# Performance work log

Measured on AMD Instinct MI355X. Metric: run time of the kernel, lower is better.

The kernel has to match this reference:

```python
import jax, jax.numpy as jnp
import numpy as np

B, S, V = 2, 336, 8      # batch, seq_len, n_vars
D, H, P = 256, 8, 96     # d_model, num_heads, pred_len
DK = D // H
OUT_CHN = 8
EPS = 1e-5


def _layernorm(x, g, b):
    mu = jnp.mean(x, axis=-1, keepdims=True)
    var = jnp.var(x, axis=-1, keepdims=True)
    return (x - mu) * jax.lax.rsqrt(var + EPS) * g + b


def _attn_ff(src, Wq, bq, Wk, bk, Wv, bv, Wo, bo, ln1_g, ln1_b):
    # src: [N, L, D]; manual MHA + residual + layernorm (dropout=0)
    N, L, _ = src.shape
    q = (src @ Wq + bq).reshape(N, L, H, DK).transpose(0, 2, 1, 3)
    k = (src @ Wk + bk).reshape(N, L, H, DK).transpose(0, 2, 1, 3)
    v = (src @ Wv + bv).reshape(N, L, H, DK).transpose(0, 2, 1, 3)
    scores = jnp.einsum('nhqd,nhkd->nhqk', q, k) / np.sqrt(DK).astype(np.float32)
    attn = jax.nn.softmax(scores, axis=-1)
    o = jnp.einsum('nhqk,nhkd->nhqd', attn, v)
    o = o.transpose(0, 2, 1, 3).reshape(N, L, D) @ Wo + bo
    return _layernorm(src + o, ln1_g, ln1_b)


def setup_inputs() -> dict:
    key = jax.random.key(0)
    ks = jax.random.split(key, 8)
    s = 1.0 / np.sqrt(D)
    return {
        'x': jax.random.normal(ks[0], (B, S, V), dtype=jnp.float32),
        'emb_w': jax.random.normal(ks[1], (1, D), dtype=jnp.float32),
        'emb_b': jnp.zeros((D,), jnp.float32),
        'Wq': jax.random.normal(ks[2], (D, D), dtype=jnp.float32) * s,
        'bq': jnp.zeros((D,), jnp.float32),
        'Wk': jax.random.normal(ks[3], (D, D), dtype=jnp.float32) * s,
        'bk': jnp.zeros((D,), jnp.float32),
        'Wv': jax.random.normal(ks[4], (D, D), dtype=jnp.float32) * s,
        'bv': jnp.zeros((D,), jnp.float32),
        'Wo': jax.random.normal(ks[5], (D, D), dtype=jnp.float32) * s,
        'bo': jnp.zeros((D,), jnp.float32),
        'ln1_g': jnp.ones((D,), jnp.float32),
        'ln1_b': jnp.zeros((D,), jnp.float32),
        'norm_g': jnp.ones((D,), jnp.float32),
        'norm_b': jnp.zeros((D,), jnp.float32),
        'proj_w': jax.random.normal(ks[6], (S * D, P), dtype=jnp.float32) / np.sqrt(S * D).astype(np.float32),
        'proj_b': jnp.zeros((P,), jnp.float32),
    }


def reference(x, emb_w, emb_b, Wq, bq, Wk, bk, Wv, bv, Wo, bo,
              ln1_g, ln1_b, norm_g, norm_b, proj_w, proj_b):
    attn_p = (Wq, bq, Wk, bk, Wv, bv, Wo, bo, ln1_g, ln1_b)
    # x: [B,S,V] -> [B,V,S] -> embed each scalar to D
    e = x.transpose(0, 2, 1)[..., None] @ emb_w + emb_b  # [B,V,S,D]
    for _ in range(10):
        # attention over time axis (shared weights)
        e = _attn_ff(e.reshape(B * V, S, D), *attn_p).reshape(B, V, S, D)
        e = _layernorm(e.transpose(0, 2, 1, 3), norm_g, norm_b)  # [B,S,V,D]
        # attention over variable axis (same weights)
        e = _attn_ff(e.reshape(B * S, V, D), *attn_p).reshape(B, S, V, D)
        e = e.transpose(0, 2, 1, 3)  # [B,V,S,D]
    out = e.reshape(B, V, S * D) @ proj_w + proj_b  # [B,V,P]
    return out.transpose(0, 2, 1)[:, :, :OUT_CHN]  # [B,P,out_chn]
```

## Files before the change

kernel.cpp:

```cpp
#include <hip/hip_runtime.h>

#define SS 336
#define VV 8
#define DD 256
#define DKK 32
#define NTOK 5376
#define NTD (NTOK * DD)
#define ATT_SCALE 0.17677669529663687f
#define LN_EPS 1e-5f

typedef _Float16 f16x8 __attribute__((ext_vector_type(8)));
typedef _Float16 f16x4v __attribute__((ext_vector_type(4)));
typedef __attribute__((ext_vector_type(4))) float f32x4;

__device__ inline _Float16 f2h(float f) { return (_Float16)f; }

__global__ __launch_bounds__(256) void k_init(
    const float* __restrict__ Wq, const float* __restrict__ Wk,
    const float* __restrict__ Wv, const float* __restrict__ Wo,
    const float* __restrict__ x, const float* __restrict__ ew,
    const float* __restrict__ eb, const float* __restrict__ PB,
    _Float16* __restrict__ WT2, float* __restrict__ E,
    _Float16* __restrict__ E16, float* __restrict__ out) {
  int bid = blockIdx.x;
  int tid = threadIdx.x;
  if (bid < 1024) {
    int z = bid >> 8;
    const float* W = (z == 0) ? Wq : (z == 1) ? Wk : (z == 2) ? Wv : Wo;
    int o = (bid & 255) * 256 + tid;
    int blk = o >> 9;
    int idx = o & 511;
    int lane = idx >> 3, j = idx & 7;
    int nt = blk >> 3, kb = blk & 7;
    int lcol = lane & 15, quad = lane >> 4;
    int n = nt * 16 + lcol;
    int k = kb * 32 + quad * 8 + j;
    WT2[(size_t)z * 65536 + o] = f2h(W[k * 256 + n]);
    if (bid == 0) {
      for (int i = tid; i < 1536; i += 256) {
        int row = i / 96, p = i - row * 96;
        out[(row >> 3) * 768 + p * 8 + (row & 7)] = PB[p];
      }
    }
  } else {
    int token = bid - 1024;
    int n = token / SS, s = token - n * SS;
    int b = n >> 3, v = n & 7;
    float xv = x[(b * SS + s) * VV + v];
    int d = tid;
    float val = fmaf(xv, ew[d], eb[d]);
    E[token * DD + d] = val;
    E16[token * DD + d] = f2h(val);
  }
}

#define KSTR 36
#define VTSTR 344
#define PSTR 72
#define QSTR 40
__global__ __launch_bounds__(512) void k_attn_time(
    const _Float16* __restrict__ Et16, const _Float16* __restrict__ Q16,
    const _Float16* __restrict__ K16, const _Float16* __restrict__ V16,
    const _Float16* __restrict__ WT2,
    const float* __restrict__ bq, const float* __restrict__ bk,
    const float* __restrict__ bv, _Float16* __restrict__ O16, int mode) {
  int qg = blockIdx.x, h = blockIdx.y, n = blockIdx.z;
  int tid = threadIdx.x;
  int wave = tid >> 6, lane = tid & 63;
  int quad = lane >> 4, lcol = lane & 15;

  __shared__ __align__(16) char SMRAW[143264];
  _Float16* Ks  = (_Float16*)SMRAW;
  _Float16* Vt  = (_Float16*)(SMRAW + 24192);
  _Float16* Qs  = (_Float16*)(SMRAW + 46240);
  _Float16* Wl  = (_Float16*)(SMRAW + 60320);
  _Float16* Ach = (_Float16*)(SMRAW + 109472);
  _Float16* PsB = (_Float16*)(mode ? SMRAW + 60320 : SMRAW + 46240);

  const size_t ebase = (size_t)(n * SS) * DD;
  const size_t base  = ebase + h * DKK;
  int qt0 = qg ? 11 : 0;
  int qtend = qg ? 21 : 11;

  const f32x4 z4 = {0.f, 0.f, 0.f, 0.f};

  if (mode) {
    {
      int h2 = h * 2;
      for (int c = tid; c < 3072; c += 512) {
        int ot = c >> 9, rest = c & 511;
        int z = (ot < 2) ? 1 : (ot < 4) ? 2 : 0;
        int nt = h2 + (ot & 1);
        *(f16x8*)&Wl[(ot << 12) + rest * 8] =
            *(const f16x8*)&WT2[(size_t)z * 65536 + nt * 4096 + rest * 8];
      }
      for (int c = tid; c < 272; c += 512) {
        if (c < 256) {
          int d = c >> 3, col = 336 + (c & 7);
          Vt[d * VTSTR + col] = (_Float16)0.f;
        } else {
          Vt[32 * VTSTR + (c - 256)] = (_Float16)0.f;
        }
      }
    }
    for (int ck = 0; ck < 6; ++ck) {
      int m0c = ck * 64;
      int nmt = (ck < 5) ? 4 : 1;
      __syncthreads();
      for (int c = tid; c < nmt * 16 * 32; c += 512) {
        int row = c >> 5, seg = c & 31;
        *(f16x8*)&Ach[row * 264 + seg * 8] =
            *(const f16x8*)&Et16[ebase + (size_t)(m0c + row) * 256 + seg * 8];
      }
      __syncthreads();
      int nU = nmt * 6;
      for (int u = wave; u < nU; u += 8) {
        int mtl = u / 6, ot = u % 6;
        int gt = ck * 4 + mtl;
        if (ot >= 4 && (gt < qt0 || gt >= qtend)) continue;
        f32x4 acc = z4;
#pragma unroll
        for (int kb = 0; kb < 8; ++kb) {
          f16x8 af = *(const f16x8*)&Ach[(mtl * 16 + lcol) * 264 + kb * 32 + quad * 8];
          f16x8 wf = *(const f16x8*)&Wl[(ot << 12) + kb * 512 + lane * 8];
          acc = __builtin_amdgcn_mfma_f32_16x16x32_f16(af, wf, acc, 0, 0, 0);
        }
        int dlo = ((ot & 1) << 4) + lcol;
        const float* bz = (ot < 2) ? bk : (ot < 4) ? bv : bq;
        float bval = bz[h * 32 + dlo];
        if (ot < 2) {
#pragma unroll
          for (int i = 0; i < 4; ++i)
            Ks[(m0c + mtl * 16 + quad * 4 + i) * KSTR + dlo] = f2h(acc[i] + bval);
        } else if (ot < 4) {
#pragma unroll
          for (int i = 0; i < 4; ++i)
            Vt[dlo * VTSTR + (m0c + mtl * 16 + quad * 4 + i)] = f2h(acc[i] + bval);
        } else {
          int ql = gt - qt0;
#pragma unroll
          for (int i = 0; i < 4; ++i)
            Qs[(ql * 16 + quad * 4 + i) * QSTR + dlo] = f2h(acc[i] + bval);
        }
      }
    }
    __syncthreads();
  } else {
    for (int c = tid; c < 1344; c += 512) {
      int row = c >> 2, part = c & 3;
      f16x8 kv = *(const f16x8*)&K16[base + (size_t)row * DD + part * 8];
      f16x4v klo = __builtin_shufflevector(kv, kv, 0, 1, 2, 3);
      f16x4v khi = __builtin_shufflevector(kv, kv, 4, 5, 6, 7);
      *(f16x4v*)&Ks[row * KSTR + part * 8] = klo;
      *(f16x4v*)&Ks[row * KSTR + part * 8 + 4] = khi;
      f16x8 vv = *(const f16x8*)&V16[base + (size_t)row * DD + part * 8];
#pragma unroll
      for (int j = 0; j < 8; ++j) Vt[(part * 8 + j) * VTSTR + row] = vv[j];
    }
    for (int c = tid; c < 272; c += 512) {
      if (c < 256) {
        int d = c >> 3, col = 336 + (c & 7);
        Vt[d * VTSTR + col] = (_Float16)0.f;
      } else {
        Vt[32 * VTSTR + (c - 256)] = (_Float16)0.f;
      }
    }
    __syncthreads();
  }

  _Float16* P = PsB + wave * (16 * PSTR);
  const f16x8 onesv = {(_Float16)1.f, (_Float16)1.f, (_Float16)1.f, (_Float16)1.f,
                       (_Float16)1.f, (_Float16)1.f, (_Float16)1.f, (_Float16)1.f};

  for (int qtile = qt0 + wave; qtile < qtend; qtile += 8) {
    int qb = qtile * 16;
    int ql = qtile - qt0;

    f16x8 qf;
    if (mode)
      qf = *(const f16x8*)&Qs[(ql * 16 + lcol) * QSTR + quad * 8];
    else
      qf = *(const f16x8*)&Q16[base + (size_t)(qb + lcol) * DD + quad * 8];
    f32x4 accA = {0.f, 0.f, 0.f, 0.f};
    f32x4 accB = {0.f, 0.f, 0.f, 0.f};
    f32x4 lacc = {0.f, 0.f, 0.f, 0.f};
    float m_[4] = {-1e30f, -1e30f, -1e30f, -1e30f};

    for (int T = 0; T < 6; ++T) {
      int k0 = T * 64;
      bool full = (T < 5);
      f32x4 s[4];
      {
        const _Float16* kp = &Ks[(k0 + lcol) * KSTR + quad * 8];
        f16x4v a0 = *(const f16x4v*)kp;
        f16x4v b0 = *(const f16x4v*)(kp + 4);
        f16x8 kf = __builtin_shufflevector(a0, b0, 0, 1, 2, 3, 4, 5, 6, 7);
        s[0] = __builtin_amdgcn_mfma_f32_16x16x32_f16(qf, kf, z4, 0, 0, 0);
      }
      if (full) {
#pragma unroll
        for (int u = 1; u < 4; ++u) {
          const _Float16* kp = &Ks[(k0 + u * 16 + lcol) * KSTR + quad * 8];
          f16x4v a0 = *(const f16x4v*)kp;
          f16x4v b0 = *(const f16x4v*)(kp + 4);
          f16x8 kf = __builtin_shufflevector(a0, b0, 0, 1, 2, 3, 4, 5, 6, 7);
          s[u] = __builtin_amdgcn_mfma_f32_16x16x32_f16(qf, kf, z4, 0, 0, 0);
        }
      } else {
        s[1] = z4; s[2] = z4; s[3] = z4;
      }
      float sc[4][4], p[4][4], corr[4];
#pragma unroll
      for (int u = 0; u < 4; ++u)
#pragma unroll
        for (int i = 0; i < 4; ++i)
          sc[u][i] = (u == 0 || full) ? s[u][i] * ATT_SCALE : -1e30f;
#pragma unroll
      for (int i = 0; i < 4; ++i) {
        float t2 = fmaxf(fmaxf(sc[0][i], sc[1][i]), fmaxf(sc[2][i], sc[3][i]));
        t2 = fmaxf(t2, __shfl_xor(t2, 1));
        t2 = fmaxf(t2, __shfl_xor(t2, 2));
        t2 = fmaxf(t2, __shfl_xor(t2, 4));
        t2 = fmaxf(t2, __shfl_xor(t2, 8));
        float nm = fmaxf(m_[i], t2);
        corr[i] = __expf(m_[i] - nm);
        m_[i] = nm;
#pragma unroll
        for (int u = 0; u < 4; ++u) p[u][i] = __expf(sc[u][i] - nm);
        accA[i] *= corr[i];
        accB[i] *= corr[i];
        lacc[i] *= corr[i];
      }
#pragma unroll
      for (int i = 0; i < 4; ++i)
#pragma unroll
        for (int u = 0; u < 4; ++u)
          P[(quad * 4 + i) * PSTR + u * 16 + lcol] = f2h(p[u][i]);
      f16x8 pf0 = *(const f16x8*)&P[lcol * PSTR + quad * 8];
      lacc = __builtin_amdgcn_mfma_f32_16x16x32_f16(pf0, onesv, lacc, 0, 0, 0);
      f16x8 va0 = *(const f16x8*)&Vt[lcol * VTSTR + k0 + quad * 8];
      f16x8 vb0 = *(const f16x8*)&Vt[(16 + lcol) * VTSTR + k0 + quad * 8];
      accA = __builtin_amdgcn_mfma_f32_16x16x32_f16(pf0, va0, accA, 0, 0, 0);
      accB = __builtin_amdgcn_mfma_f32_16x16x32_f16(pf0, vb0, accB, 0, 0, 0);
      if (full) {
        f16x8 pf1 = *(const f16x8*)&P[lcol * PSTR + 32 + quad * 8];
        lacc = __builtin_amdgcn_mfma_f32_16x16x32_f16(pf1, onesv, lacc, 0, 0, 0);
        f16x8 va1 = *(const f16x8*)&Vt[lcol * VTSTR + k0 + 32 + quad * 8];
        f16x8 vb1 = *(const f16x8*)&Vt[(16 + lcol) * VTSTR + k0 + 32 + quad * 8];
        accA = __builtin_amdgcn_mfma_f32_16x16x32_f16(pf1, va1, accA, 0, 0, 0);
        accB = __builtin_amdgcn_mfma_f32_16x16x32_f16(pf1, vb1, accB, 0, 0, 0);
      }
    }

#pragma unroll
    for (int i = 0; i < 4; ++i) {
      float inv = 1.f / lacc[i];
      P[(quad * 4 + i) * PSTR + lcol] = f2h(accA[i] * inv);
      P[(quad * 4 + i) * PSTR + 16 + lcol] = f2h(accB[i] * inv);
    }
    int row = lane >> 2, seg = lane & 3;
    f16x8 ov = *(const f16x8*)&P[row * PSTR + seg * 8];
    *(f16x8*)&O16[base + (size_t)(qb + row) * DD + seg * 8] = ov;
  }
}

__global__ __launch_bounds__(512) void k_mega_var(
    const _Float16* __restrict__ AO16, const _Float16* __restrict__ WT2,
    const float* __restrict__ bq, const float* __restrict__ bk,
    const float* __restrict__ bv, const float* __restrict__ bo,
    const float* __restrict__ g1, const float* __restrict__ c1,
    const float* __restrict__ gn, const float* __restrict__ bn,
    float* __restrict__ Etime, _Float16* __restrict__ Q16,
    _Float16* __restrict__ K16, _Float16* __restrict__ V16, int doqkv) {
  int tid = threadIdx.x;
  int wave = tid >> 6, lane = tid & 63;
  int quad = lane >> 4, lcol = lane & 15;

  __shared__ int rmapS[32];
  __shared__ _Float16 Af[32 * 264];
  __shared__ float Cf[32 * 260];
  __shared__ _Float16 QKVs[32 * 776];

  if (tid < 32) {
    int r2 = blockIdx.x * 32 + tid;
    int n_idx = r2 >> 3, v = r2 & 7;
    int b = n_idx / SS, s = n_idx - b * SS;
    rmapS[tid] = (b * VV + v) * SS + s;
  }
  __syncthreads();

  {
    int row = tid >> 4, seg = tid & 15;
    const _Float16* src = AO16 + (size_t)rmapS[row] * DD + seg * 16;
    _Float16* dst = Af + row * 264 + seg * 16;
    *(f16x8*)(dst) = *(const f16x8*)(src);
    *(f16x8*)(dst + 8) = *(const f16x8*)(src + 8);
  }
  __syncthreads();

  const _Float16* WoF = WT2 + (size_t)3 * 65536;

  {
    f32x4 acc[2][2] = {};
    for (int kb = 0; kb < 8; ++kb) {
      int k0 = kb * 32;
      f16x8 af0 = *(const f16x8*)&Af[lcol * 264 + k0 + quad * 8];
      f16x8 af1 = *(const f16x8*)&Af[(16 + lcol) * 264 + k0 + quad * 8];
#pragma unroll
      for (int nt = 0; nt < 2; ++nt) {
        f16x8 bfr = *(const f16x8*)&WoF[((wave * 2 + nt) * 8 + kb) * 512 + lane * 8];
        acc[0][nt] = __builtin_amdgcn_mfma_f32_16x16x32_f16(af0, bfr, acc[0][nt], 0, 0, 0);
        acc[1][nt] = __builtin_amdgcn_mfma_f32_16x16x32_f16(af1, bfr, acc[1][nt], 0, 0, 0);
      }
    }
#pragma unroll
    for (int mt = 0; mt < 2; ++mt) {
#pragma unroll
      for (int i = 0; i < 4; ++i) {
        int row = mt * 16 + quad * 4 + i;
        size_t rb = (size_t)rmapS[row] * 256;
#pragma unroll
        for (int nt = 0; nt < 2; ++nt) {
          int col = (wave * 2 + nt) * 16 + lcol;
          Cf[row * 260 + col] = acc[mt][nt][i] + bo[col] + Etime[rb + col];
        }
      }
    }
  }
  __syncthreads();

  {
    int row = tid >> 4, c0 = (tid & 15) * 16;
    float v[16];
#pragma unroll
    for (int j = 0; j < 16; ++j) v[j] = Cf[row * 260 + c0 + j];
#pragma unroll
    for (int pass = 0; pass < 2; ++pass) {
      const float* gg = pass ? gn : g1;
      const float* bb = pass ? bn : c1;
      float s = 0.f, q = 0.f;
#pragma unroll
      for (int j = 0; j < 16; ++j) { s += v[j]; q = fmaf(v[j], v[j], q); }
      s += __shfl_xor(s, 1); q += __shfl_xor(q, 1);
      s += __shfl_xor(s, 2); q += __shfl_xor(q, 2);
      s += __shfl_xor(s, 4); q += __shfl_xor(q, 4);
      s += __shfl_xor(s, 8); q += __shfl_xor(q, 8);
      float mu = s * (1.0f / 256.0f);
      float rs = rsqrtf(q * (1.0f / 256.0f) - mu * mu + LN_EPS);
#pragma unroll
      for (int j = 0; j < 16; ++j)
        v[j] = fmaf((v[j] - mu) * rs, gg[c0 + j], bb[c0 + j]);
    }
#pragma unroll
    for (int j = 0; j < 16; ++j) Cf[row * 260 + c0 + j] = v[j];
#pragma unroll
    for (int j8 = 0; j8 < 2; ++j8) {
      f16x8 h;
#pragma unroll
      for (int jj = 0; jj < 8; ++jj) h[jj] = f2h(v[j8 * 8 + jj]);
      *(f16x8*)&Af[row * 264 + c0 + j8 * 8] = h;
    }
  }
  __syncthreads();

  {
    f32x4 acc[2][6] = {};
    for (int kb = 0; kb < 8; ++kb) {
      int k0 = kb * 32;
      f16x8 af0 = *(const f16x8*)&Af[lcol * 264 + k0 + quad * 8];
      f16x8 af1 = *(const f16x8*)&Af[(16 + lcol) * 264 + k0 + quad * 8];
#pragma unroll
      for (int j = 0; j < 6; ++j) {
        int ntg = wave * 6 + j;
        f16x8 bfr = *(const f16x8*)&WT2[(size_t)(ntg * 8 + kb) * 512 + lane * 8];
        acc[0][j] = __builtin_amdgcn_mfma_f32_16x16x32_f16(af0, bfr, acc[0][j], 0, 0, 0);
        acc[1][j] = __builtin_amdgcn_mfma_f32_16x16x32_f16(af1, bfr, acc[1][j], 0, 0, 0);
      }
    }
#pragma unroll
    for (int j = 0; j < 6; ++j) {
      int ntg = wave * 6 + j;
      int colb = ntg * 16;
      int z = colb >> 8, coln = (colb & 255) + lcol;
      const float* bz = (z == 0) ? bq : (z == 1) ? bk : bv;
      float bval = bz[coln];
#pragma unroll
      for (int mt = 0; mt < 2; ++mt) {
#pragma unroll
        for (int i = 0; i < 4; ++i)
          QKVs[(mt * 16 + quad * 4 + i) * 776 + colb + lcol] = f2h(acc[mt][j][i] + bval);
      }
    }
  }
  __syncthreads();

  {
    int half = tid & 1, qi = (tid >> 1) & 7, h = (tid >> 4) & 7, ng = tid >> 7;
    int d0 = h * 32 + half * 16;
    const _Float16* Qp = &QKVs[(ng * 8 + qi) * 776 + d0];
    float qv[16];
#pragma unroll
    for (int j8 = 0; j8 < 2; ++j8) {
      f16x8 t = *(const f16x8*)(Qp + j8 * 8);
#pragma unroll
      for (int jj = 0; jj < 8; ++jj) qv[j8 * 8 + jj] = (float)t[jj];
    }
    float sc[8];
#pragma unroll
    for (int k = 0; k < 8; ++k) {
      const _Float16* Kp = &QKVs[(ng * 8 + k) * 776 + 256 + d0];
      float s = 0.f;
#pragma unroll
      for (int j8 = 0; j8 < 2; ++j8) {
        f16x8 t = *(const f16x8*)(Kp + j8 * 8);
#pragma unroll
        for (int jj = 0; jj < 8; ++jj) s = fmaf(qv[j8 * 8 + jj], (float)t[jj], s);
      }
      sc[k] = s;
    }
#pragma unroll
    for (int k = 0; k < 8; ++k)
      sc[k] = (sc[k] + __shfl_xor(sc[k], 1)) * ATT_SCALE;
    float mx = sc[0];
#pragma unroll
    for (int k = 1; k < 8; ++k) mx = fmaxf(mx, sc[k]);
    float ps = 0.f;
#pragma unroll
    for (int k = 0; k < 8; ++k) { sc[k] = __expf(sc[k] - mx); ps += sc[k]; }
    float inv = 1.f / ps;
    float ov[16];
#pragma unroll
    for (int j = 0; j < 16; ++j) ov[j] = 0.f;
#pragma unroll
    for (int k = 0; k < 8; ++k) {
      const _Float16* Vp = &QKVs[(ng * 8 + k) * 776 + 512 + d0];
      float p = sc[k];
#pragma unroll
      for (int j8 = 0; j8 < 2; ++j8) {
        f16x8 t = *(const f16x8*)(Vp + j8 * 8);
#pragma unroll
        for (int jj = 0; jj < 8; ++jj)
          ov[j8 * 8 + jj] = fmaf(p, (float)t[jj], ov[j8 * 8 + jj]);
      }
    }
    _Float16* Op = &Af[(ng * 8 + qi) * 264 + d0];
#pragma unroll
    for (int j8 = 0; j8 < 2; ++j8) {
      f16x8 hh;
#pragma unroll
      for (int jj = 0; jj < 8; ++jj) hh[jj] = f2h(ov[j8 * 8 + jj] * inv);
      *(f16x8*)(Op + j8 * 8) = hh;
    }
  }
  __syncthreads();

  {
    f32x4 acc[2][2] = {};
    for (int kb = 0; kb < 8; ++kb) {
      int k0 = kb * 32;
      f16x8 af0 = *(const f16x8*)&Af[lcol * 264 + k0 + quad * 8];
      f16x8 af1 = *(const f16x8*)&Af[(16 + lcol) * 264 + k0 + quad * 8];
#pragma unroll
      for (int nt = 0; nt < 2; ++nt) {
        f16x8 bfr = *(const f16x8*)&WoF[((wave * 2 + nt) * 8 + kb) * 512 + lane * 8];
        acc[0][nt] = __builtin_amdgcn_mfma_f32_16x16x32_f16(af0, bfr, acc[0][nt], 0, 0, 0);
        acc[1][nt] = __builtin_amdgcn_mfma_f32_16x16x32_f16(af1, bfr, acc[1][nt], 0, 0, 0);
      }
    }
#pragma unroll
    for (int mt = 0; mt < 2; ++mt) {
#pragma unroll
      for (int i = 0; i < 4; ++i) {
        int row = mt * 16 + quad * 4 + i;
#pragma unroll
        for (int nt = 0; nt < 2; ++nt) {
          int col = (wave * 2 + nt) * 16 + lcol;
          Cf[row * 260 + col] = acc[mt][nt][i] + bo[col] + Cf[row * 260 + col];
        }
      }
    }
  }
  __syncthreads();

  {
    int row = tid >> 4, c0 = (tid & 15) * 16;
    float v[16];
#pragma unroll
    for (int j = 0; j < 16; ++j) v[j] = Cf[row * 260 + c0 + j];
    float s = 0.f, q = 0.f;
#pragma unroll
    for (int j = 0; j < 16; ++j) { s += v[j]; q = fmaf(v[j], v[j], q); }
    s += __shfl_xor(s, 1); q += __shfl_xor(q, 1);
    s += __shfl_xor(s, 2); q += __shfl_xor(q, 2);
    s += __shfl_xor(s, 4); q += __shfl_xor(q, 4);
    s += __shfl_xor(s, 8); q += __shfl_xor(q, 8);
    float mu = s * (1.0f / 256.0f);
    float rs = rsqrtf(q * (1.0f / 256.0f) - mu * mu + LN_EPS);
#pragma unroll
    for (int j = 0; j < 16; ++j)
      v[j] = fmaf((v[j] - mu) * rs, g1[c0 + j], c1[c0 + j]);
    size_t rb = (size_t)rmapS[row] * 256 + c0;
#pragma unroll
    for (int j4 = 0; j4 < 4; ++j4) {
      float4 f4 = make_float4(v[j4 * 4], v[j4 * 4 + 1], v[j4 * 4 + 2], v[j4 * 4 + 3]);
      *(float4*)&Etime[rb + j4 * 4] = f4;
    }
#pragma unroll
    for (int j8 = 0; j8 < 2; ++j8) {
      f16x8 hh;
#pragma unroll
      for (int jj = 0; jj < 8; ++jj) hh[jj] = f2h(v[j8 * 8 + jj]);
      *(f16x8*)&Af[row * 264 + c0 + j8 * 8] = hh;
    }
  }
  __syncthreads();

  if (doqkv) {
    f32x4 acc[2][6] = {};
    for (int kb = 0; kb < 8; ++kb) {
      int k0 = kb * 32;
      f16x8 af0 = *(const f16x8*)&Af[lcol * 264 + k0 + quad * 8];
      f16x8 af1 = *(const f16x8*)&Af[(16 + lcol) * 264 + k0 + quad * 8];
#pragma unroll
      for (int j = 0; j < 6; ++j) {
        int ntg = wave * 6 + j;
        f16x8 bfr = *(const f16x8*)&WT2[(size_t)(ntg * 8 + kb) * 512 + lane * 8];
        acc[0][j] = __builtin_amdgcn_mfma_f32_16x16x32_f16(af0, bfr, acc[0][j], 0, 0, 0);
        acc[1][j] = __builtin_amdgcn_mfma_f32_16x16x32_f16(af1, bfr, acc[1][j], 0, 0, 0);
      }
    }
#pragma unroll
    for (int j = 0; j < 6; ++j) {
      int ntg = wave * 6 + j;
      int colb = ntg * 16;
      int z = colb >> 8, coln = (colb & 255) + lcol;
      const float* bz = (z == 0) ? bq : (z == 1) ? bk : bv;
      _Float16* Hd = (z == 0) ? Q16 : (z == 1) ? K16 : V16;
      float bval = bz[coln];
#pragma unroll
      for (int mt = 0; mt < 2; ++mt) {
#pragma unroll
        for (int i = 0; i < 4; ++i) {
          int row = mt * 16 + quad * 4 + i;
          Hd[(size_t)rmapS[row] * 256 + coln] = f2h(acc[mt][j][i] + bval);
        }
      }
    }
  }
}

__global__ __launch_bounds__(384) void k_proj(
    const float* __restrict__ E, const float* __restrict__ PW,
    float* __restrict__ out) {
  __shared__ float Es[16][336];
  __shared__ float sm[16][1536];
  int tid = threadIdx.x;
  int kc0 = blockIdx.x * 336;
  for (int idx = tid; idx < 1344; idx += 384) {
    int row = idx / 84, kk4 = idx % 84;
    *(float4*)&Es[row][kk4 * 4] =
        *(const float4*)&E[(size_t)row * 86016 + kc0 + kk4 * 4];
  }
  __syncthreads();
  int g = tid / 24, p4 = tid % 24;
  float4 acc[16];
#pragma unroll
  for (int r = 0; r < 16; ++r) acc[r] = make_float4(0.f, 0.f, 0.f, 0.f);
  int kbase = kc0 + g * 21;
#pragma unroll 7
  for (int j = 0; j < 21; ++j) {
    float4 w = *(const float4*)&PW[(size_t)(kbase + j) * 96 + p4 * 4];
#pragma unroll
    for (int r = 0; r < 16; ++r) {
      float e = Es[r][g * 21 + j];
      acc[r].x = fmaf(e, w.x, acc[r].x);
      acc[r].y = fmaf(e, w.y, acc[r].y);
      acc[r].z = fmaf(e, w.z, acc[r].z);
      acc[r].w = fmaf(e, w.w, acc[r].w);
    }
  }
#pragma unroll
  for (int r = 0; r < 16; ++r)
    *(float4*)&sm[g][r * 96 + p4 * 4] = acc[r];
  __syncthreads();
  for (int o = tid; o < 1536; o += 384) {
    float s = 0.f;
#pragma unroll
    for (int g2 = 0; g2 < 16; ++g2) s += sm[g2][o];
    int row = o / 96, p = o - row * 96;
    atomicAdd(&out[(row >> 3) * 768 + p * 8 + (row & 7)], s);
  }
}

extern "C" void kernel_launch(void* const* d_in, const int* in_sizes, int n_in,
                              void* d_out, int out_size, void* d_ws,
                              size_t ws_size, hipStream_t stream) {
  const float* x     = (const float*)d_in[0];
  const float* emb_w = (const float*)d_in[1];
  const float* emb_b = (const float*)d_in[2];
  const float* Wq = (const float*)d_in[3];
  const float* bq = (const float*)d_in[4];
  const float* Wk = (const float*)d_in[5];
  const float* bk = (const float*)d_in[6];
  const float* Wv = (const float*)d_in[7];
  const float* bv = (const float*)d_in[8];
  const float* Wo = (const float*)d_in[9];
  const float* bo = (const float*)d_in[10];
  const float* g1 = (const float*)d_in[11];
  const float* b1 = (const float*)d_in[12];
  const float* gn = (const float*)d_in[13];
  const float* bn = (const float*)d_in[14];
  const float* PW = (const float*)d_in[15];
  const float* PB = (const float*)d_in[16];
  float* out = (float*)d_out;

  float* ws = (float*)d_ws;
  float* Etime   = ws;
  _Float16* Et16 = (_Float16*)(ws + (size_t)NTD);
  _Float16* Q16  = (_Float16*)(ws + (size_t)NTD + NTD / 2);
  _Float16* K16  = Q16 + (size_t)NTD;
  _Float16* V16  = K16 + (size_t)NTD;
  _Float16* AO16 = V16 + (size_t)NTD;
  _Float16* WT2  = AO16 + (size_t)NTD;

  k_init<<<6400, 256, 0, stream>>>(Wq, Wk, Wv, Wo, x, emb_w, emb_b, PB,
                                   WT2, Etime, Et16, out);
  for (int it = 0; it < 10; ++it) {
    k_attn_time<<<dim3(2, 8, 16), 512, 0, stream>>>(
        Et16, Q16, K16, V16, WT2, bq, bk, bv, AO16, (it == 0) ? 1 : 0);
    k_mega_var<<<168, 512, 0, stream>>>(
        AO16, WT2, bq, bk, bv, bo, g1, b1, gn, bn, Etime,
        Q16, K16, V16, (it < 9) ? 1 : 0);
  }
  k_proj<<<256, 384, 0, stream>>>(Etime, PW, out);
}
```

Before: 615.8 us.

## Run final projection with fp16 MFMA using pre-swizzled projection weights

The init kernel now converts proj_w into fp16 in an MFMA-friendly fragment layout. The last variable-attention pass also writes an fp16 copy of the final activations. The fp32 FMA projection kernel is replaced by one using 16x16x32 fp16 MFMA over 256-wide K chunks, with atomic accumulation into the output. This cuts FP32 ALU work and halves the memory read for the 8.6M-element projection weight on each call. The cost is a weight conversion on every call, which reads the full fp32 weight, and reduced precision over a long reduction.

```diff
diff --git a/kernel.cpp b/kernel.cpp
--- a/kernel.cpp
+++ b/kernel.cpp
@@ -20,8 +20,10 @@
     const float* __restrict__ Wv, const float* __restrict__ Wo,
     const float* __restrict__ x, const float* __restrict__ ew,
     const float* __restrict__ eb, const float* __restrict__ PB,
+    const float* __restrict__ PW,
     _Float16* __restrict__ WT2, float* __restrict__ E,
-    _Float16* __restrict__ E16, float* __restrict__ out) {
+    _Float16* __restrict__ E16, _Float16* __restrict__ PWF,
+    float* __restrict__ out) {
   int bid = blockIdx.x;
   int tid = threadIdx.x;
   if (bid < 1024) {
@@ -42,7 +44,7 @@
         out[(row >> 3) * 768 + p * 8 + (row & 7)] = PB[p];
       }
     }
-  } else {
+  } else if (bid < 6400) {
     int token = bid - 1024;
     int n = token / SS, s = token - n * SS;
     int b = n >> 3, v = n & 7;
@@ -51,6 +53,18 @@
     float val = fmaf(xv, ew[d], eb[d]);
     E[token * DD + d] = val;
     E16[token * DD + d] = f2h(val);
+  } else {
+    int idx = (bid - 6400) * 256 + tid;
+    int ktile = idx / 384;
+    int rem = idx - ktile * 384;
+    int nt = rem >> 6, lane = rem & 63;
+    int quad = lane >> 4, lcol = lane & 15;
+    int k0 = ktile * 32 + quad * 8;
+    int n = nt * 16 + lcol;
+    f16x8 w;
+#pragma unroll
+    for (int j = 0; j < 8; ++j) w[j] = f2h(PW[(size_t)(k0 + j) * 96 + n]);
+    *(f16x8*)&PWF[(size_t)idx * 8] = w;
   }
 }
 
@@ -271,7 +285,8 @@
     const float* __restrict__ g1, const float* __restrict__ c1,
     const float* __restrict__ gn, const float* __restrict__ bn,
     float* __restrict__ Etime, _Float16* __restrict__ Q16,
-    _Float16* __restrict__ K16, _Float16* __restrict__ V16, int doqkv) {
+    _Float16* __restrict__ K16, _Float16* __restrict__ V16,
+    _Float16* __restrict__ Et16, int doqkv) {
   int tid = threadIdx.x;
   int wave = tid >> 6, lane = tid & 63;
   int quad = lane >> 4, lcol = lane & 15;
@@ -511,6 +526,7 @@
 #pragma unroll
       for (int jj = 0; jj < 8; ++jj) hh[jj] = f2h(v[j8 * 8 + jj]);
       *(f16x8*)&Af[row * 264 + c0 + j8 * 8] = hh;
+      if (!doqkv) *(f16x8*)&Et16[rb + j8 * 8] = hh;
     }
   }
   __syncthreads();
@@ -549,46 +565,46 @@
   }
 }
 
-__global__ __launch_bounds__(384) void k_proj(
-    const float* __restrict__ E, const float* __restrict__ PW,
+__global__ __launch_bounds__(512) void k_proj(
+    const _Float16* __restrict__ Et16, const _Float16* __restrict__ PWF,
     float* __restrict__ out) {
-  __shared__ float Es[16][336];
-  __shared__ float sm[16][1536];
+  __shared__ _Float16 Ets[16 * 264];
+  __shared__ _Float16 PWFs[8 * 6 * 512];
   int tid = threadIdx.x;
-  int kc0 = blockIdx.x * 336;
-  for (int idx = tid; idx < 1344; idx += 384) {
-    int row = idx / 84, kk4 = idx % 84;
-    *(float4*)&Es[row][kk4 * 4] =
-        *(const float4*)&E[(size_t)row * 86016 + kc0 + kk4 * 4];
-  }
-  __syncthreads();
-  int g = tid / 24, p4 = tid % 24;
-  float4 acc[16];
-#pragma unroll
-  for (int r = 0; r < 16; ++r) acc[r] = make_float4(0.f, 0.f, 0.f, 0.f);
-  int kbase = kc0 + g * 21;
-#pragma unroll 7
-  for (int j = 0; j < 21; ++j) {
-    float4 w = *(const float4*)&PW[(size_t)(kbase + j) * 96 + p4 * 4];
-#pragma unroll
-    for (int r = 0; r < 16; ++r) {
-      float e = Es[r][g * 21 + j];
-      acc[r].x = fmaf(e, w.x, acc[r].x);
-      acc[r].y = fmaf(e, w.y, acc[r].y);
-      acc[r].z = fmaf(e, w.z, acc[r].z);
-      acc[r].w = fmaf(e, w.w, acc[r].w);
-    }
-  }
-#pragma unroll
-  for (int r = 0; r < 16; ++r)
-    *(float4*)&sm[g][r * 96 + p4 * 4] = acc[r];
-  __syncthreads();
-  for (int o = tid; o < 1536; o += 384) {
-    float s = 0.f;
-#pragma unroll
-    for (int g2 = 0; g2 < 16; ++g2) s += sm[g2][o];
-    int row = o / 96, p = o - row * 96;
-    atomicAdd(&out[(row >> 3) * 768 + p * 8 + (row & 7)], s);
+  int wave = tid >> 6, lane = tid & 63;
+  int quad = lane >> 4, lcol = lane & 15;
+  int kt0 = blockIdx.x * 8;
+  size_t kc0 = (size_t)kt0 * 32;
+
+  {
+    int r = tid >> 5, seg = tid & 31;
+    *(f16x8*)&Ets[r * 264 + seg * 8] =
+        *(const f16x8*)&Et16[(size_t)r * 86016 + kc0 + seg * 8];
+  }
+  {
+    const _Float16* src = PWF + (size_t)kt0 * 6 * 512;
+#pragma unroll
+    for (int i = 0; i < 6; ++i) {
+      int g = i * 512 + tid;
+      *(f16x8*)&PWFs[g * 8] = *(const f16x8*)&src[(size_t)g * 8];
+    }
+  }
+  __syncthreads();
+
+  if (wave < 6) {
+    f32x4 acc = {0.f, 0.f, 0.f, 0.f};
+#pragma unroll
+    for (int kt = 0; kt < 8; ++kt) {
+      f16x8 af = *(const f16x8*)&Ets[lcol * 264 + kt * 32 + quad * 8];
+      f16x8 bf = *(const f16x8*)&PWFs[((kt * 6 + wave) << 9) + lane * 8];
+      acc = __builtin_amdgcn_mfma_f32_16x16x32_f16(af, bf, acc, 0, 0, 0);
+    }
+    int col = wave * 16 + lcol;
+#pragma unroll
+    for (int i = 0; i < 4; ++i) {
+      int r = quad * 4 + i;
+      atomicAdd(&out[(r >> 3) * 768 + col * 8 + (r & 7)], acc[i]);
+    }
   }
 }
 
@@ -622,15 +638,16 @@
   _Float16* V16  = K16 + (size_t)NTD;
   _Float16* AO16 = V16 + (size_t)NTD;
   _Float16* WT2  = AO16 + (size_t)NTD;
-
-  k_init<<<6400, 256, 0, stream>>>(Wq, Wk, Wv, Wo, x, emb_w, emb_b, PB,
-                                   WT2, Etime, Et16, out);
+  _Float16* PWF  = WT2 + 4 * 65536;
+
+  k_init<<<10432, 256, 0, stream>>>(Wq, Wk, Wv, Wo, x, emb_w, emb_b, PB, PW,
+                                    WT2, Etime, Et16, PWF, out);
   for (int it = 0; it < 10; ++it) {
     k_attn_time<<<dim3(2, 8, 16), 512, 0, stream>>>(
         Et16, Q16, K16, V16, WT2, bq, bk, bv, AO16, (it == 0) ? 1 : 0);
     k_mega_var<<<168, 512, 0, stream>>>(
         AO16, WT2, bq, bk, bv, bo, g1, b1, gn, bn, Etime,
-        Q16, K16, V16, (it < 9) ? 1 : 0);
-  }
-  k_proj<<<256, 384, 0, stream>>>(Etime, PW, out);
+        Q16, K16, V16, Et16, (it < 9) ? 1 : 0);
+  }
+  k_proj<<<336, 512, 0, stream>>>(Et16, PWF, out);
 }
```

New measurement: 578.6 us. -6.0%, faster.
